# Kernel tuning notes

Measured on AMD Instinct MI355X. Metric: run time of the kernel, lower is better.

Reference implementation:

```python
import jax, jax.numpy as jnp
import numpy as np

T = 8          # hardcoded timesteps in QNetwork
TAU = 2.0      # spikingjelly LIFNode default tau
SG_ALPHA = 4.0 # sigmoid surrogate alpha (default)

@jax.custom_vjp
def spike_fn(x):
    # heaviside with sigmoid surrogate gradient (spikingjelly default)
    return (x >= 0.0).astype(x.dtype)

def _spike_fwd(x):
    return spike_fn(x), x

def _spike_bwd(x, g):
    s = jax.nn.sigmoid(SG_ALPHA * x)
    return (g * SG_ALPHA * s * (1.0 - s),)

spike_fn.defvjp(_spike_fwd, _spike_bwd)

def lif_multistep(x_seq, v_th):
    """Multi-step LIF over leading T dim. x_seq: (T, B, H).
    v starts at 0 because functional.reset_net is called before each frame.
    Returns (spikes (T,B,H), final membrane potential v (B,H))."""
    def step(v, x):
        v = v + (x - v) / TAU          # decay_input=True, v_reset=0
        s = spike_fn(v - v_th)
        v = v * (1.0 - s)              # hard reset to 0
        return v, s
    v0 = jnp.zeros_like(x_seq[0])
    v_final, spikes = jax.lax.scan(step, v0, x_seq)
    return spikes, v_final

def setup_inputs() -> dict:
    key = jax.random.key(0)
    ks = jax.random.split(key, 10)
    B, FRAMES, S, H, A = 2048, 8, 128, 512, 4
    init_w = 0.003
    def lin(k, out_f, in_f):
        k1, k2 = jax.random.split(k)
        bound = 1.0 / np.sqrt(in_f)
        W = jax.random.uniform(k1, (out_f, in_f), jnp.float32, -bound, bound)
        b = jax.random.uniform(k2, (out_f,), jnp.float32, -bound, bound)
        return W, b
    W_i1, b_i1 = lin(ks[0], H, S)
    W_h1, b_h1 = lin(ks[1], H, H)
    W_i2, b_i2 = lin(ks[2], H, H)
    W_h2, b_h2 = lin(ks[3], H, H)
    # fc weights: nn.init.uniform_(-init_w, init_w)
    W_f1 = jax.random.uniform(ks[4], (H, H + A), jnp.float32, -init_w, init_w)
    b_f1 = jax.random.uniform(ks[5], (H,), jnp.float32, -init_w, init_w)
    W_f2 = jax.random.uniform(ks[6], (1, H), jnp.float32, -init_w, init_w)
    b_f2 = jax.random.uniform(ks[7], (1,), jnp.float32, -init_w, init_w)
    state = jax.random.normal(ks[8], (B, FRAMES, S), jnp.float32)
    action = jax.random.normal(ks[9], (B, A), jnp.float32)
    return dict(state=state, action=action,
                W_i1=W_i1, b_i1=b_i1, W_h1=W_h1, b_h1=b_h1,
                W_i2=W_i2, b_i2=b_i2, W_h2=W_h2, b_h2=b_h2,
                W_f1=W_f1, b_f1=b_f1, W_f2=W_f2, b_f2=b_f2)

def reference(state, action, W_i1, b_i1, W_h1, b_h1, W_i2, b_i2, W_h2, b_h2,
              W_f1, b_f1, W_f2, b_f2):
    B = state.shape[0]
    H = W_h1.shape[0]
    # state is repeated identically across T, so i2h of rnn1 can be computed once
    # per frame and broadcast across T (same math as the original).
    ih1 = jnp.einsum('bfs,hs->fbh', state, W_i1) + b_i1   # (F, B, H)

    def frame_step1(h1, ih_f):
        # h1: (T, B, H) spikes from previous frame; ih_f: (B, H)
        x = ih_f[None] + h1 @ W_h1.T + b_h1               # (T, B, H)
        spikes, _ = lif_multistep(x, 1.0)
        return spikes, spikes

    h1_0 = jnp.zeros((T, B, H), state.dtype)
    _, h1_seq = jax.lax.scan(frame_step1, h1_0, ih1)      # (F, T, B, H)

    def frame_step2(h2, inp_f):
        # inp_f: (T, B, H) rnn1 spikes for this frame
        x = inp_f @ W_i2.T + b_i2 + h2 @ W_h2.T + b_h2
        spikes, v_final = lif_multistep(x, 999.0)
        return spikes, v_final

    h2_0 = jnp.zeros((T, B, H), state.dtype)
    _, v_seq = jax.lax.scan(frame_step2, h2_0, h1_seq)    # (F, B, H)

    v_last = v_seq[-1]                                    # rnn_output[:, -1]: (B, H)
    x = jnp.concatenate([v_last, action], axis=1)         # (B, H + A)
    q = jax.nn.relu(x @ W_f1.T + b_f1) @ W_f2.T + b_f2    # (B, 1)
    return q
```

## Files before the change

### kernel.cpp

```cpp
#include <hip/hip_runtime.h>
#include <stdint.h>

typedef unsigned long long u64;
typedef unsigned int uint;
typedef unsigned short u16;

#define NB   2048
#define NF   8
#define NT   8
#define NS   128
#define NH   512
#define NAct 4
#define HEAD_B 8
#define TPB  512
#define LW   516

__global__ void k_prep(const float* __restrict__ W_i1,
                       const float* __restrict__ W_h1,
                       const float* __restrict__ W_i2,
                       const float* __restrict__ W_f1,
                       float* __restrict__ Wti1s,
                       float* __restrict__ Wt1s,
                       float* __restrict__ Wt2s,
                       float* __restrict__ Wtf1)
{
    int idx = blockIdx.x * 256 + threadIdx.x;
    if (idx < NS * NH) {
        int s = idx >> 9, h = idx & 511;
        Wti1s[idx] = W_i1[h * NS + s];
    }
    if (idx < NH * NH) {
        int k = idx >> 9, h = idx & 511;
        Wt1s[idx] = W_h1[h * NH + k];
        Wt2s[idx] = W_i2[h * NH + k];
    }
    if (idx < NH) {
        Wt1s[NH * NH + idx] = 0.f;
        Wt2s[NH * NH + idx] = 0.f;
    }
    if (idx < (NH + NAct) * NH) {
        int j = idx / NH, hh = idx % NH;
        Wtf1[idx] = W_f1[hh * (NH + NAct) + j];
    }
}

__device__ __forceinline__ void extract_lists(int lane, int t,
                                              const u64 (*mask)[8],
                                              u16 (*s_idx)[LW],
                                              uint* s_cnt)
{
    if (lane < 8) {
        const int w = lane;
        u64 m = mask[t][w];
        int base = 0;
        for (int w2 = 0; w2 < w; ++w2) base += (int)__popcll(mask[t][w2]);
        uint kbase = (uint)(w << 6);
        while (m) {
            int kb = __builtin_ctzll(m);
            m &= m - 1;
            s_idx[t][base++] = (u16)(kbase + kb);
        }
        if (w == 7) {
            uint cnt = (uint)base;
            uint pad = (4u - (cnt & 3u)) & 3u;
            for (uint p = 0; p < pad; ++p) s_idx[t][cnt + p] = (u16)NH;
            s_cnt[t] = cnt + pad;
        }
    }
}

#define LOAD4(P0,P1,P2,P3, base)                                           \
    {                                                                      \
        uint2 qv = *(const uint2*)(lst + (base));                          \
        uint o0 = __builtin_amdgcn_readfirstlane((qv.x & 0xFFFFu) << 11);  \
        uint o1 = __builtin_amdgcn_readfirstlane((qv.x >> 16) << 11);      \
        uint o2 = __builtin_amdgcn_readfirstlane((qv.y & 0xFFFFu) << 11);  \
        uint o3 = __builtin_amdgcn_readfirstlane((qv.y >> 16) << 11);      \
        P0 = *(const float*)(tb + (o0 + hoff));                            \
        P1 = *(const float*)(tb + (o1 + hoff));                            \
        P2 = *(const float*)(tb + (o2 + hoff));                            \
        P3 = *(const float*)(tb + (o3 + hoff));                            \
    }

#define ADD4(P0,P1,P2,P3)                                                 \
    a += (double)P0; a += (double)P1; a += (double)P2; a += (double)P3;

__device__ __forceinline__ double gather4(const char* tb, const u16* lst,
                                          uint n, uint hoff)
{
    double a = 0.0;
    if (!n) return a;
    const uint m = n >> 2;
    float A0, A1, A2, A3, B0, B1, B2, B3;
    LOAD4(A0, A1, A2, A3, 0)
    uint c = 1;
    for (; c + 1 < m; c += 2) {
        LOAD4(B0, B1, B2, B3, c << 2)
        ADD4(A0, A1, A2, A3)
        LOAD4(A0, A1, A2, A3, (c + 1) << 2)
        ADD4(B0, B1, B2, B3)
    }
    if (c < m) {
        LOAD4(B0, B1, B2, B3, c << 2)
        ADD4(A0, A1, A2, A3)
        ADD4(B0, B1, B2, B3)
    } else {
        ADD4(A0, A1, A2, A3)
    }
    return a;
}

__global__ __launch_bounds__(TPB) void k_snn(
    const float* __restrict__ state,
    const float* __restrict__ Wti1s,
    const float* __restrict__ b_i1,
    const float* __restrict__ Wt1s,
    const float* __restrict__ b_h1,
    const float* __restrict__ Wt2s,
    const float* __restrict__ b_i2,
    const float* __restrict__ b_h2,
    float* __restrict__ vlast)
{
    const int b    = blockIdx.x;
    const int tid  = threadIdx.x;
    const int lane = tid & 63;
    const int wv   = tid >> 6;

    __shared__ double s_state[NF * NS];
    __shared__ alignas(16) u16 s_idx[NT][LW];
    __shared__ u64  s_mask[2][NT][8];
    __shared__ uint s_cnt[NT];

    {
        const float2* sp2 = (const float2*)(state + (size_t)b * NF * NS);
        float2 v2 = sp2[tid];
        s_state[tid * 2 + 0] = (double)v2.x;
        s_state[tid * 2 + 1] = (double)v2.y;
    }
    if (tid < 128) ((u64*)s_mask)[tid] = 0ull;
    __syncthreads();

    double ih0[NF];
#pragma unroll
    for (int f = 0; f < NF; ++f) ih0[f] = 0.0;
    for (int s = 0; s < NS; ++s) {
        double w = (double)Wti1s[s * NH + tid];
#pragma unroll
        for (int f = 0; f < NF; ++f)
            ih0[f] = fma(s_state[f * NS + s], w, ih0[f]);
    }
    {
        double bb = (double)b_i1[tid];
#pragma unroll
        for (int f = 0; f < NF; ++f) ih0[f] += bb;
    }
    const double bh1v = (double)b_h1[tid];
    const char*  w1b  = (const char*)Wt1s;
    const uint   hoff = (uint)tid * 4u;

    for (int f = 0; f < NF; ++f) {
        const int rb = f & 1, wb = rb ^ 1;
        __syncthreads();
        extract_lists(lane, wv, s_mask[rb], s_idx, s_cnt);
        __syncthreads();

        const double ihc = ih0[0];
        double v = 0.0;
        for (int t = 0; t < NT; ++t) {
            double a = gather4(w1b, s_idx[t], s_cnt[t], hoff);
            double x = (ihc + a) + bh1v;
            v = v + (x - v) * 0.5;
            bool sp = (v - 1.0) >= 0.0;
            u64 m = __ballot(sp);
            if (lane == 0) s_mask[wb][t][wv] = m;
            if (sp) v = 0.0;
        }
#pragma unroll
        for (int j = 0; j < NF - 1; ++j) ih0[j] = ih0[j + 1];
    }

    __syncthreads();
    extract_lists(lane, wv, s_mask[0], s_idx, s_cnt);
    __syncthreads();

    {
        const char* w2b = (const char*)Wt2s;
        const double bi = (double)b_i2[tid];
        const double bg = (double)b_h2[tid];
        double v = 0.0;
        for (int t = 0; t < NT; ++t) {
            double a = gather4(w2b, s_idx[t], s_cnt[t], hoff);
            double x = (a + bi) + bg;
            v = v + (x - v) * 0.5;
            if ((v - 999.0) >= 0.0) v = 0.0;
        }
        vlast[(size_t)b * NH + tid] = (float)v;
    }
}

__global__ __launch_bounds__(512) void k_head(
    const float* __restrict__ vlast,
    const float* __restrict__ action,
    const float* __restrict__ Wtf1,
    const float* __restrict__ b_f1,
    const float* __restrict__ W_f2,
    const float* __restrict__ b_f2,
    float* __restrict__ q)
{
    const int h    = threadIdx.x;
    const int lane = h & 63;
    const int wv   = h >> 6;
    const int b0   = blockIdx.x * HEAD_B;

    __shared__ float s_x[HEAD_B][NH + NAct];
    for (int i = h; i < HEAD_B * NH; i += 512) {
        int bi = i / NH, j = i % NH;
        s_x[bi][j] = vlast[(size_t)(b0 + bi) * NH + j];
    }
    if (h < HEAD_B * NAct) {
        int bi = h / NAct, j = h % NAct;
        s_x[bi][NH + j] = action[(b0 + bi) * NAct + j];
    }
    __syncthreads();

    float acc[HEAD_B] = {0, 0, 0, 0, 0, 0, 0, 0};
#pragma unroll 4
    for (int j = 0; j < NH + NAct; ++j) {
        float w = Wtf1[j * NH + h];
#pragma unroll
        for (int i = 0; i < HEAD_B; ++i)
            acc[i] = fmaf(s_x[i][j], w, acc[i]);
    }

    const float bf = b_f1[h];
    const float w2 = W_f2[h];
    float p[HEAD_B];
#pragma unroll
    for (int i = 0; i < HEAD_B; ++i) {
        float hv = acc[i] + bf;
        hv = hv < 0.f ? 0.f : hv;
        p[i] = hv * w2;
    }
#pragma unroll
    for (int off = 32; off; off >>= 1) {
#pragma unroll
        for (int i = 0; i < HEAD_B; ++i)
            p[i] += __shfl_down(p[i], off);
    }
    __shared__ float red[8][HEAD_B];
    if (lane == 0) {
#pragma unroll
        for (int i = 0; i < HEAD_B; ++i) red[wv][i] = p[i];
    }
    __syncthreads();
    if (h < HEAD_B) {
        float s = 0.f;
#pragma unroll
        for (int w = 0; w < 8; ++w) s += red[w][h];
        q[b0 + h] = s + b_f2[0];
    }
}

extern "C" void kernel_launch(void* const* d_in, const int* in_sizes, int n_in,
                              void* d_out, int out_size, void* d_ws, size_t ws_size,
                              hipStream_t stream)
{
    const float* state  = (const float*)d_in[0];
    const float* action = (const float*)d_in[1];
    const float* W_i1   = (const float*)d_in[2];
    const float* b_i1   = (const float*)d_in[3];
    const float* W_h1   = (const float*)d_in[4];
    const float* b_h1   = (const float*)d_in[5];
    const float* W_i2   = (const float*)d_in[6];
    const float* b_i2   = (const float*)d_in[7];
    const float* b_h2   = (const float*)d_in[9];
    const float* W_f1   = (const float*)d_in[10];
    const float* b_f1   = (const float*)d_in[11];
    const float* W_f2   = (const float*)d_in[12];
    const float* b_f2   = (const float*)d_in[13];

    char* ws = (char*)d_ws;
    float* Wti1s = (float*)(ws);
    float* Wt1s  = (float*)(ws + 262144);
    float* Wt2s  = (float*)(ws + 1312768);
    float* Wtf1  = (float*)(ws + 2363392);
    float* vlast = (float*)(ws + 3420160);

    k_prep<<<((NH + NAct) * NH + 255) / 256, 256, 0, stream>>>(
        W_i1, W_h1, W_i2, W_f1, Wti1s, Wt1s, Wt2s, Wtf1);

    k_snn<<<NB, TPB, 0, stream>>>(state, Wti1s, b_i1, Wt1s, b_h1,
                                  Wt2s, b_i2, b_h2, vlast);

    k_head<<<NB / HEAD_B, 512, 0, stream>>>(vlast, action, Wtf1, b_f1,
                                            W_f2, b_f2, (float*)d_out);
}
```

Baseline: 227.2 us.

## Gather union of spiking neurons across timesteps once, apply per-timestep bitmask

Instead of building a separate spike index list for each of the 8 timesteps and gathering weight rows per timestep, the kernel builds one list over the union of neurons that spiked at any timestep. Each entry packs the row offset with an 8-bit timestep mask. Each weight row is then loaded once and added conditionally into 8 double accumulators. This cuts redundant global weight loads when the same neurons spike at several timesteps. The cost is 8 live double accumulators, per-element branchy masked adds, and a serial list build done by only 8 threads.

New measurement: 338.2 us. 48.8% more time.

```diff
diff --git a/kernel.cpp b/kernel.cpp
--- a/kernel.cpp
+++ b/kernel.cpp
@@ -3,7 +3,6 @@
 
 typedef unsigned long long u64;
 typedef unsigned int uint;
-typedef unsigned short u16;
 
 #define NB   2048
 #define NF   8
@@ -13,7 +12,7 @@
 #define NAct 4
 #define HEAD_B 8
 #define TPB  512
-#define LW   516
+#define LW   520
 
 __global__ void k_prep(const float* __restrict__ W_i1,
                        const float* __restrict__ W_h1,
@@ -44,70 +43,71 @@
     }
 }
 
-__device__ __forceinline__ void extract_lists(int lane, int t,
+__device__ __forceinline__ void extract_union(int tid,
                                               const u64 (*mask)[8],
-                                              u16 (*s_idx)[LW],
+                                              uint* s_idx,
                                               uint* s_cnt)
 {
-    if (lane < 8) {
-        const int w = lane;
-        u64 m = mask[t][w];
+    if (tid < 8) {
+        const int w = tid;
+        u64 u = 0;
+#pragma unroll
+        for (int t = 0; t < NT; ++t) u |= mask[t][w];
         int base = 0;
-        for (int w2 = 0; w2 < w; ++w2) base += (int)__popcll(mask[t][w2]);
+        for (int w2 = 0; w2 < w; ++w2) {
+            u64 uw = 0;
+#pragma unroll
+            for (int t = 0; t < NT; ++t) uw |= mask[t][w2];
+            base += (int)__popcll(uw);
+        }
         uint kbase = (uint)(w << 6);
-        while (m) {
-            int kb = __builtin_ctzll(m);
-            m &= m - 1;
-            s_idx[t][base++] = (u16)(kbase + kb);
+        while (u) {
+            int kb = __builtin_ctzll(u);
+            u &= u - 1;
+            uint tm = 0;
+#pragma unroll
+            for (int t = 0; t < NT; ++t)
+                tm |= (uint)((mask[t][w] >> kb) & 1ull) << t;
+            s_idx[base++] = ((kbase + (uint)kb) << 11) | tm;
         }
         if (w == 7) {
             uint cnt = (uint)base;
             uint pad = (4u - (cnt & 3u)) & 3u;
-            for (uint p = 0; p < pad; ++p) s_idx[t][cnt + p] = (u16)NH;
-            s_cnt[t] = cnt + pad;
-        }
-    }
-}
-
-#define LOAD4(P0,P1,P2,P3, base)                                           \
-    {                                                                      \
-        uint2 qv = *(const uint2*)(lst + (base));                          \
-        uint o0 = __builtin_amdgcn_readfirstlane((qv.x & 0xFFFFu) << 11);  \
-        uint o1 = __builtin_amdgcn_readfirstlane((qv.x >> 16) << 11);      \
-        uint o2 = __builtin_amdgcn_readfirstlane((qv.y & 0xFFFFu) << 11);  \
-        uint o3 = __builtin_amdgcn_readfirstlane((qv.y >> 16) << 11);      \
-        P0 = *(const float*)(tb + (o0 + hoff));                            \
-        P1 = *(const float*)(tb + (o1 + hoff));                            \
-        P2 = *(const float*)(tb + (o2 + hoff));                            \
-        P3 = *(const float*)(tb + (o3 + hoff));                            \
-    }
-
-#define ADD4(P0,P1,P2,P3)                                                 \
-    a += (double)P0; a += (double)P1; a += (double)P2; a += (double)P3;
-
-__device__ __forceinline__ double gather4(const char* tb, const u16* lst,
-                                          uint n, uint hoff)
-{
-    double a = 0.0;
-    if (!n) return a;
-    const uint m = n >> 2;
-    float A0, A1, A2, A3, B0, B1, B2, B3;
-    LOAD4(A0, A1, A2, A3, 0)
-    uint c = 1;
-    for (; c + 1 < m; c += 2) {
-        LOAD4(B0, B1, B2, B3, c << 2)
-        ADD4(A0, A1, A2, A3)
-        LOAD4(A0, A1, A2, A3, (c + 1) << 2)
-        ADD4(B0, B1, B2, B3)
-    }
-    if (c < m) {
-        LOAD4(B0, B1, B2, B3, c << 2)
-        ADD4(A0, A1, A2, A3)
-        ADD4(B0, B1, B2, B3)
-    } else {
-        ADD4(A0, A1, A2, A3)
-    }
-    return a;
+            for (uint p = 0; p < pad; ++p) s_idx[cnt + p] = ((uint)NH << 11);
+            *s_cnt = cnt + pad;
+        }
+    }
+}
+
+#define APPLY_TM(vv, dd)                                           \
+    {                                                              \
+        _Pragma("unroll")                                          \
+        for (int t = 0; t < NT; ++t)                               \
+            if (vv & (1u << t)) acc[t] += dd;                      \
+    }
+
+__device__ __forceinline__ void gather_union(const char* tb, const uint* lst,
+                                             uint n, uint hoff, double* acc)
+{
+    for (uint i = 0; i < n; i += 4) {
+        uint4 qv = *(const uint4*)(lst + i);
+        uint v0 = __builtin_amdgcn_readfirstlane(qv.x);
+        uint v1 = __builtin_amdgcn_readfirstlane(qv.y);
+        uint v2 = __builtin_amdgcn_readfirstlane(qv.z);
+        uint v3 = __builtin_amdgcn_readfirstlane(qv.w);
+        float w0 = *(const float*)(tb + ((v0 & 0xFFFFF800u) + hoff));
+        float w1 = *(const float*)(tb + ((v1 & 0xFFFFF800u) + hoff));
+        float w2 = *(const float*)(tb + ((v2 & 0xFFFFF800u) + hoff));
+        float w3 = *(const float*)(tb + ((v3 & 0xFFFFF800u) + hoff));
+        double d0 = (double)w0;
+        APPLY_TM(v0, d0)
+        double d1 = (double)w1;
+        APPLY_TM(v1, d1)
+        double d2 = (double)w2;
+        APPLY_TM(v2, d2)
+        double d3 = (double)w3;
+        APPLY_TM(v3, d3)
+    }
 }
 
 __global__ __launch_bounds__(TPB) void k_snn(
@@ -127,9 +127,9 @@
     const int wv   = tid >> 6;
 
     __shared__ double s_state[NF * NS];
-    __shared__ alignas(16) u16 s_idx[NT][LW];
+    __shared__ alignas(16) uint s_idx[LW];
     __shared__ u64  s_mask[2][NT][8];
-    __shared__ uint s_cnt[NT];
+    __shared__ uint s_cnt;
 
     {
         const float2* sp2 = (const float2*)(state + (size_t)b * NF * NS);
@@ -161,14 +161,19 @@
     for (int f = 0; f < NF; ++f) {
         const int rb = f & 1, wb = rb ^ 1;
         __syncthreads();
-        extract_lists(lane, wv, s_mask[rb], s_idx, s_cnt);
+        extract_union(tid, s_mask[rb], s_idx, &s_cnt);
         __syncthreads();
+
+        double acc[NT];
+#pragma unroll
+        for (int t = 0; t < NT; ++t) acc[t] = 0.0;
+        gather_union(w1b, s_idx, s_cnt, hoff, acc);
 
         const double ihc = ih0[0];
         double v = 0.0;
+#pragma unroll
         for (int t = 0; t < NT; ++t) {
-            double a = gather4(w1b, s_idx[t], s_cnt[t], hoff);
-            double x = (ihc + a) + bh1v;
+            double x = (ihc + acc[t]) + bh1v;
             v = v + (x - v) * 0.5;
             bool sp = (v - 1.0) >= 0.0;
             u64 m = __ballot(sp);
@@ -180,17 +185,22 @@
     }
 
     __syncthreads();
-    extract_lists(lane, wv, s_mask[0], s_idx, s_cnt);
+    extract_union(tid, s_mask[0], s_idx, &s_cnt);
     __syncthreads();
 
     {
         const char* w2b = (const char*)Wt2s;
+        double acc[NT];
+#pragma unroll
+        for (int t = 0; t < NT; ++t) acc[t] = 0.0;
+        gather_union(w2b, s_idx, s_cnt, hoff, acc);
+
         const double bi = (double)b_i2[tid];
         const double bg = (double)b_h2[tid];
         double v = 0.0;
+#pragma unroll
         for (int t = 0; t < NT; ++t) {
-            double a = gather4(w2b, s_idx[t], s_cnt[t], hoff);
-            double x = (a + bi) + bg;
+            double x = (acc[t] + bi) + bg;
             v = v + (x - v) * 0.5;
             if ((v - 999.0) >= 0.0) v = 0.0;
         }
```
